# Performance work log

Hardware: AMD Instinct MI355X
Metric: run time of the kernel (lower is better)

The kernel has to match this reference:

```python
import jax, jax.numpy as jnp
import numpy as np

VARIANCES = jnp.array([0.1, 0.1, 0.2, 0.2], jnp.float32)
TOTAL_LABELS = 81
MAX_TOTAL = 200        # max_total_size (also max_output_size_per_class)
SCORE_T = 0.5          # score_threshold
IOU_T = 0.5            # tf combined_non_max_suppression default iou_threshold


def setup_inputs() -> dict:
    key = jax.random.key(0)
    k1, k2, k3, k4 = jax.random.split(key, 4)
    B, N, C = 8, 1000, TOTAL_LABELS
    # valid normalized RoIs: y1,x1 in [0,0.7), h,w in [0.01,0.31)
    yx1 = jax.random.uniform(k1, (B, N, 2), jnp.float32) * 0.7
    hw = jax.random.uniform(k2, (B, N, 2), jnp.float32) * 0.3 + 0.01
    roi_bboxes = jnp.concatenate([yx1, yx1 + hw], axis=-1)  # [y1,x1,y2,x2]
    pred_deltas = jax.random.normal(k3, (B, N, C * 4), jnp.float32) * 0.5
    pred_label_probs = jax.random.uniform(k4, (B, N, C), jnp.float32)
    return {"roi_bboxes": roi_bboxes, "pred_deltas": pred_deltas,
            "pred_label_probs": pred_label_probs}


def _decode(rois, deltas):
    # rois: [..., 4] (y1,x1,y2,x2); deltas: [..., 4] (dy,dx,dh,dw)
    h = rois[..., 2] - rois[..., 0]
    w = rois[..., 3] - rois[..., 1]
    cy = rois[..., 0] + 0.5 * h
    cx = rois[..., 1] + 0.5 * w
    ncy = deltas[..., 0] * h + cy
    ncx = deltas[..., 1] * w + cx
    nh = jnp.exp(deltas[..., 2]) * h
    nw = jnp.exp(deltas[..., 3]) * w
    return jnp.stack([ncy - 0.5 * nh, ncx - 0.5 * nw,
                      ncy + 0.5 * nh, ncx + 0.5 * nw], axis=-1)


def _nms_lane(boxes, scores):
    # greedy per-class NMS over one (batch, class) lane. boxes [N,4], scores [N]
    N = boxes.shape[0]
    order = jnp.argsort(-scores)
    b = boxes[order]
    s = scores[order]
    area = (b[:, 2] - b[:, 0]) * (b[:, 3] - b[:, 1])
    idx = jnp.arange(N)

    def body(i, keep):
        bi = b[i]
        iy1 = jnp.maximum(bi[0], b[:, 0])
        ix1 = jnp.maximum(bi[1], b[:, 1])
        iy2 = jnp.minimum(bi[2], b[:, 2])
        ix2 = jnp.minimum(bi[3], b[:, 3])
        inter = jnp.maximum(iy2 - iy1, 0.0) * jnp.maximum(ix2 - ix1, 0.0)
        iou = inter / (area[i] + area - inter + 1e-8)
        suppress = keep[i] & (iou > IOU_T) & (idx > i)
        return keep & ~suppress

    keep0 = s > SCORE_T                       # score filtering before NMS
    keep = jax.lax.fori_loop(0, N, body, keep0)
    keep = keep & (jnp.cumsum(keep) <= MAX_TOTAL)  # max_output_size_per_class
    return b, jnp.where(keep, s, 0.0)          # boxes in score order, masked scores


def _forward(roi_bboxes, pred_deltas, pred_label_probs):
    B, N, _ = pred_deltas.shape
    C = TOTAL_LABELS
    deltas = pred_deltas.reshape(B, N, C, 4) * VARIANCES
    boxes = _decode(roi_bboxes[:, :, None, :], deltas)          # [B,N,C,4]
    bg = jnp.argmax(pred_label_probs, axis=-1)[..., None] == 0  # background rows
    scores = jnp.where(bg, 0.0, pred_label_probs)               # [B,N,C]

    boxes_t = boxes.transpose(0, 2, 1, 3)   # [B,C,N,4]
    scores_t = scores.transpose(0, 2, 1)    # [B,C,N]
    b_s, s_s = jax.vmap(jax.vmap(_nms_lane))(boxes_t, scores_t)

    flat_s = s_s.reshape(B, C * N)
    flat_b = b_s.reshape(B, C * N, 4)
    cls = jnp.broadcast_to(jnp.arange(C)[:, None], (C, N)).reshape(C * N)

    top_s, top_i = jax.lax.top_k(flat_s, MAX_TOTAL)             # combined top-k
    top_b = jnp.take_along_axis(flat_b, top_i[..., None], axis=1)
    top_c = cls[top_i]

    valid = top_s > 0.0
    final_b = jnp.clip(jnp.where(valid[..., None], top_b, 0.0), 0.0, 1.0)
    final_c = jnp.where(valid, top_c, 0).astype(jnp.float32)
    final_s = jnp.where(valid, top_s, 0.0)
    return final_b, final_c, final_s


def reference(roi_bboxes, pred_deltas, pred_label_probs):
    return _forward(roi_bboxes, pred_deltas, pred_label_probs)
```

## Files before the change

### kernel.cpp

```cpp
#include <hip/hip_runtime.h>

#define NROI 1000
#define NCLS 81
#define NB   8
#define NLANE (NB*NCLS)
#define MAXM 1024
#define MAXKEEP 200
#define SCORE_T 0.5f
#define NT 512
#define NW 8
#define HBITS 13
#define HSIZE (1<<HBITS)
#define SCAP 1024

typedef unsigned long long u64;
typedef unsigned int u32;


__device__ __forceinline__ void decode_box(const float* __restrict__ roi,
                                           const float* __restrict__ dl,
                                           float& oy1, float& ox1,
                                           float& oy2, float& ox2) {
#pragma clang fp contract(off)
  float y1 = roi[0], x1 = roi[1], y2 = roi[2], x2 = roi[3];
  float h = y2 - y1;
  float w = x2 - x1;
  float cy = y1 + 0.5f * h;
  float cx = x1 + 0.5f * w;
  float d0 = dl[0] * 0.1f;
  float d1 = dl[1] * 0.1f;
  float d2 = dl[2] * 0.2f;
  float d3 = dl[3] * 0.2f;
  float ncy = d0 * h + cy;
  float ncx = d1 * w + cx;
  float nh = expf(d2) * h;
  float nw = expf(d3) * w;
  oy1 = ncy - 0.5f * nh;
  ox1 = ncx - 0.5f * nw;
  oy2 = ncy + 0.5f * nh;
  ox2 = ncx + 0.5f * nw;
}

__device__ __forceinline__ float area_f(float4 bx) {
#pragma clang fp contract(off)
  return (bx.z - bx.x) * (bx.w - bx.y);
}

__device__ __forceinline__ bool hit_f(float4 bi, float ia, float4 bj, float ja) {
#pragma clang fp contract(off)
  float yy1 = fmaxf(bi.x, bj.x);
  float xx1 = fmaxf(bi.y, bj.y);
  float yy2 = fminf(bi.z, bj.z);
  float xx2 = fminf(bi.w, bj.w);
  float ih = fmaxf(yy2 - yy1, 0.0f);
  float iw = fmaxf(xx2 - xx1, 0.0f);
  float inter = ih * iw;
  float den = ia + ja;
  den = den - inter;
  den = den + 1e-8f;
  return (inter + inter) > den;
}

__device__ __forceinline__ u64 pack_key(u32 sbits, int flat, int n) {
  return ((u64)sbits << 32) | ((u64)(131071 - flat) << 15) | ((u64)n << 5);
}

__global__ __launch_bounds__(256) void bg_kernel(const float* __restrict__ probs,
                                                 int* __restrict__ bg) {
  int row = blockIdx.x * 4 + (threadIdx.x >> 6);
  int lane = threadIdx.x & 63;
  if (row >= NB * NROI) return;
  const float* p = probs + (size_t)row * NCLS;
  float m = -1e30f;
  for (int idx = 1 + lane; idx < NCLS; idx += 64) m = fmaxf(m, p[idx]);
  for (int off = 32; off; off >>= 1) m = fmaxf(m, __shfl_xor(m, off));
  if (lane == 0) bg[row] = (p[0] >= m) ? 1 : 0;
}

__global__ __launch_bounds__(NT) void gather_nms_kernel(
    const float* __restrict__ roi, const float* __restrict__ deltas,
    const float* __restrict__ probs, const int* __restrict__ bg,
    int* __restrict__ keep_count, u64* __restrict__ lane_key,
    int* __restrict__ bhist) {
  int lane = (blockIdx.x % 8) * NCLS + blockIdx.x / 8;
  int b = lane / NCLS, c = lane % NCLS;
  int tid = threadIdx.x;
  int w = tid >> 6, l = tid & 63;

  __shared__ alignas(16) char smem[26624];
  float4* sbox   = (float4*)smem;
  u64*    skeyU  = (u64*)smem;
  u64*    skeyB  = (u64*)(smem + 8192);
  u64*    skey   = (u64*)(smem + 16384);
  int*    bcnt   = (int*)(smem + 24576);
  int*    bstart = (int*)(smem + 25600);
  __shared__ u64 hmask8[NW][64];
  __shared__ u64 suppm8[NW];
  __shared__ u64 keepmask[16];
  __shared__ int scount, segbase[16];

  if (tid == 0) scount = 0;
  if (tid < 256) bcnt[tid] = 0;
  __syncthreads();

  for (int base_n = 0; base_n < NROI; base_n += NT) {
    int n = base_n + tid;
    bool cand = false;
    float s = 0.0f;
    if (n < NROI) {
      int row = b * NROI + n;
      s = probs[(size_t)row * NCLS + c];
      cand = (s > SCORE_T) && (bg[row] == 0);
    }
    u64 bal = __ballot(cand);
    int wb = 0;
    if (l == 0) wb = atomicAdd(&scount, (int)__popcll(bal));
    wb = __shfl(wb, 0);
    if (cand) {
      int off = (int)__popcll(bal & ((1ull << l) - 1ull));
      u32 sb = __float_as_uint(s);
      skeyU[wb + off] = ((u64)sb << 32) | (u64)(0xFFFFFFFFu - (u32)n);
      atomicAdd(&bcnt[(sb >> 15) & 255], 1);
    }
  }
  __syncthreads();
  int M = scount;
  int nchunks = (M + 63) >> 6;

  if (w == 0) {
    int d0 = 4 * l, d1 = d0 + 1, d2 = d0 + 2, d3 = d0 + 3;
    int c0 = bcnt[255 - d0], c1 = bcnt[255 - d1];
    int c2 = bcnt[255 - d2], c3 = bcnt[255 - d3];
    int t = c0 + c1 + c2 + c3;
    int inc = t;
    for (int off = 1; off < 64; off <<= 1) {
      int v = __shfl_up(inc, off);
      if (l >= off) inc += v;
    }
    int excl = inc - t;
    int s0 = excl, s1 = excl + c0, s2 = excl + c0 + c1, s3 = excl + c0 + c1 + c2;
    bcnt[255 - d0] = s0; bstart[255 - d0] = s0;
    bcnt[255 - d1] = s1; bstart[255 - d1] = s1;
    bcnt[255 - d2] = s2; bstart[255 - d2] = s2;
    bcnt[255 - d3] = s3; bstart[255 - d3] = s3;
  }
  __syncthreads();

  for (int p = tid; p < M; p += NT) {
    u64 k = skeyU[p];
    int bkt = (int)((k >> 47) & 255);
    int pos = atomicAdd(&bcnt[bkt], 1);
    skeyB[pos] = k;
  }
  __syncthreads();

  for (int p = tid; p < M; p += NT) {
    u64 k = skeyB[p];
    int bkt = (int)((k >> 47) & 255);
    int st = bstart[bkt], en = bcnt[bkt];
    int r = st;
    for (int q = st; q < en; ++q) r += (skeyB[q] > k) ? 1 : 0;
    skey[r] = k;
  }
  if (tid < 16) {
    int rem = M - (tid << 6);
    keepmask[tid] = (rem >= 64) ? ~0ull : ((rem <= 0) ? 0ull : ((1ull << rem) - 1ull));
  }
  __syncthreads();

  if (w == 7 && nchunks > 0) {
    u64 k = skey[l];
    int nn = (int)(0xFFFFFFFFu - (u32)(k & 0xFFFFFFFFull));
    int row = b * NROI + ((l < M) ? nn : 0);
    float by1, bx1, by2, bx2;
    decode_box(roi + (size_t)row * 4, deltas + ((size_t)row * NCLS + c) * 4,
               by1, bx1, by2, bx2);
    sbox[l] = make_float4(by1, bx1, by2, bx2);
  }
  __syncthreads();

  int kc = 0;
  const u64 stridemask = 0x0101010101010101ull << w;
  const u64 low = (1ull << l) - 1ull;
  for (int ck = 0; ck < nchunks; ++ck) {
    int start = ck << 6;
    float4 bj = sbox[start + l];
    float ja = area_f(bj);

    {
      u64 part = 0;
#pragma unroll
      for (int r = 0; r < 8; ++r) {
        int i = (w << 3) + r;
        float4 bi = sbox[start + i];
        float ia = area_f(bi);
        if (hit_f(bi, ia, bj, ja)) part |= (1ull << i);
      }
      hmask8[w][l] = part;
    }

    {
      bool supp = false;
      for (int q = 0; q < ck; ++q) {
        u64 mq = keepmask[q] & stridemask;
        while (mq) {
          int i = __ffsll((unsigned long long)mq) - 1;
          mq &= mq - 1;
          float4 bi = sbox[(q << 6) + i];
          float ia = area_f(bi);
          supp |= hit_f(bi, ia, bj, ja);
        }
      }
      u64 sb = __ballot(supp);
      if (l == 0) suppm8[w] = sb;
    }

    if (w == 7 && ck + 1 < nchunks) {
      int p = ((ck + 1) << 6) + l;
      u64 k = skey[p];
      int nn = (int)(0xFFFFFFFFu - (u32)(k & 0xFFFFFFFFull));
      int row = b * NROI + ((p < M) ? nn : 0);
      float by1, bx1, by2, bx2;
      decode_box(roi + (size_t)row * 4, deltas + ((size_t)row * NCLS + c) * 4,
                 by1, bx1, by2, bx2);
      sbox[p] = make_float4(by1, bx1, by2, bx2);
    }
    __syncthreads();

    u64 rowm = hmask8[0][l] | hmask8[1][l] | hmask8[2][l] | hmask8[3][l]
             | hmask8[4][l] | hmask8[5][l] | hmask8[6][l] | hmask8[7][l];
    u64 sall = suppm8[0] | suppm8[1] | suppm8[2] | suppm8[3]
             | suppm8[4] | suppm8[5] | suppm8[6] | suppm8[7];
    int rem0 = M - start;
    u64 alive = (rem0 >= 64) ? ~0ull : ((rem0 <= 0) ? 0ull : ((1ull << rem0) - 1ull));
    u64 und = alive & ~sall;
    u64 kept = 0;
    while (und) {
      bool isu = (und >> l) & 1;
      bool su = isu && ((rowm & kept & low) != 0ull);
      bool ke = isu && ((rowm & (kept | und) & low) == 0ull);
      u64 sm = __ballot(su);
      u64 km2 = __ballot(ke);
      kept |= km2;
      und &= ~(sm | km2);
    }
    if (tid == 0) keepmask[ck] = kept;
    kc += (int)__popcll(kept);
    if (kc >= MAXKEEP) break;
    __syncthreads();
  }
  __syncthreads();

  if (tid < 16) {
    int acc = 0;
    for (int i = 0; i < tid; ++i) acc += (int)__popcll(keepmask[i]);
    segbase[tid] = acc;
  }
  __syncthreads();
  int total = segbase[15] + (int)__popcll(keepmask[15]);
  for (int s = 0; s < 2; ++s) {
    int seg = (w << 1) + s;
    u64 word = keepmask[seg];
    int p = (seg << 6) + l;
    if ((word >> l) & 1) {
      int rank = segbase[seg] + (int)__popcll(word & ((1ull << l) - 1ull));
      if (rank < MAXKEEP) {
        u64 k = skey[p];
        u32 sbits = (u32)(k >> 32);
        int n = (int)(0xFFFFFFFFu - (u32)(k & 0xFFFFFFFFull));
        lane_key[(size_t)lane * MAXKEEP + rank] = pack_key(sbits, c * NROI + p, n);
        atomicAdd(&bhist[b * HSIZE + (int)((sbits >> 10) & (HSIZE - 1))], 1);
      }
    }
  }
  if (tid == 0) keep_count[lane] = min(total, MAXKEEP);
}

__global__ __launch_bounds__(512) void merge_kernel(
    const float* __restrict__ roi, const float* __restrict__ deltas,
    const int* __restrict__ keep_count, const u64* __restrict__ lane_key,
    const int* __restrict__ bhist,
    float* __restrict__ out_b, float* __restrict__ out_c, float* __restrict__ out_s) {
  int b = blockIdx.x;
  int tid = threadIdx.x;
  int w = tid >> 6, l = tid & 63;

  __shared__ int hist[HSIZE];
  __shared__ int csum[256];
  __shared__ int cnts[NCLS];
  __shared__ int tb_sh, scnt_sh;
  __shared__ u64 surv[SCAP];

  for (int i = tid; i < HSIZE; i += 512) hist[i] = bhist[b * HSIZE + i];
  for (int i = tid; i < NCLS; i += 512) cnts[i] = keep_count[b * NCLS + i];
  if (tid == 0) { tb_sh = 0; scnt_sh = 0; }
  __syncthreads();

  int base = tid * 32;
  if (tid < 256) {
    int psum = 0;
    for (int i = 0; i < 32; ++i) psum += hist[base + i];
    csum[tid] = psum;
  }
  __syncthreads();
  if (w == 0) {
    int c0 = csum[4 * l], c1 = csum[4 * l + 1], c2 = csum[4 * l + 2], c3 = csum[4 * l + 3];
    int t = c0 + c1 + c2 + c3;
    int acc = t;
    for (int off = 1; off < 64; off <<= 1) {
      int v = __shfl_down(acc, off);
      if (l + off < 64) acc += v;
    }
    int below = acc - t;
    csum[4 * l + 3] = below + c3;
    csum[4 * l + 2] = below + c3 + c2;
    csum[4 * l + 1] = below + c3 + c2 + c1;
    csum[4 * l + 0] = below + t;
  }
  __syncthreads();
  if (tid < 256) {
    int acc = (tid < 255) ? csum[tid + 1] : 0;
    int local_tb = -1;
    for (int i = 31; i >= 0; --i) {
      acc += hist[base + i];
      if (acc >= MAXKEEP && local_tb < 0) local_tb = base + i;
    }
    if (local_tb >= 0) atomicMax(&tb_sh, local_tb);
  }
  __syncthreads();
  int tb = tb_sh;

  for (int s = tid; s < NCLS * MAXKEEP; s += 512) {
    int c = s / MAXKEEP, h = s % MAXKEEP;
    if (h < cnts[c]) {
      u64 k = lane_key[((size_t)(b * NCLS + c)) * MAXKEEP + h];
      u32 sb = (u32)(k >> 32);
      if ((int)((sb >> 10) & (HSIZE - 1)) >= tb) {
        int pos = atomicAdd(&scnt_sh, 1);
        if (pos < SCAP) surv[pos] = k;
      }
    }
  }
  __syncthreads();
  int scnt = min(scnt_sh, SCAP);
  int size = 2;
  while (size < scnt) size <<= 1;
  for (int i = scnt + tid; i < size; i += 512) surv[i] = 0ull;
  __syncthreads();

  for (int k2 = 2; k2 <= size; k2 <<= 1) {
    for (int j = k2 >> 1; j > 0; j >>= 1) {
      for (int i = tid; i < size; i += 512) {
        int ixj = i ^ j;
        if (ixj > i) {
          u64 a = surv[i], bb = surv[ixj];
          bool swp = ((i & k2) == 0) ? (a < bb) : (a > bb);
          if (swp) { surv[i] = bb; surv[ixj] = a; }
        }
      }
      __syncthreads();
    }
  }

  for (int t = tid; t < MAXKEEP; t += 512) {
    size_t ob = ((size_t)b * MAXKEEP + t) * 4;
    if (t < scnt) {
      u64 k = surv[t];
      int flat = 131071 - (int)((k >> 15) & 0x1FFFF);
      int c = flat / NROI;
      int n = (int)((k >> 5) & 0x3FF);
      int row = b * NROI + n;
      float by1, bx1, by2, bx2;
      decode_box(roi + (size_t)row * 4, deltas + ((size_t)row * NCLS + c) * 4,
                 by1, bx1, by2, bx2);
      out_b[ob + 0] = fminf(fmaxf(by1, 0.0f), 1.0f);
      out_b[ob + 1] = fminf(fmaxf(bx1, 0.0f), 1.0f);
      out_b[ob + 2] = fminf(fmaxf(by2, 0.0f), 1.0f);
      out_b[ob + 3] = fminf(fmaxf(bx2, 0.0f), 1.0f);
      out_c[b * MAXKEEP + t] = (float)c;
      out_s[b * MAXKEEP + t] = __uint_as_float((u32)(k >> 32));
    } else {
      out_b[ob + 0] = 0.0f; out_b[ob + 1] = 0.0f;
      out_b[ob + 2] = 0.0f; out_b[ob + 3] = 0.0f;
      out_c[b * MAXKEEP + t] = 0.0f;
      out_s[b * MAXKEEP + t] = 0.0f;
    }
  }
}

extern "C" void kernel_launch(void* const* d_in, const int* in_sizes, int n_in,
                              void* d_out, int out_size, void* d_ws, size_t ws_size,
                              hipStream_t stream) {
  const float* roi    = (const float*)d_in[0];
  const float* deltas = (const float*)d_in[1];
  const float* probs  = (const float*)d_in[2];

  char* ws = (char*)d_ws;
  int* bg         = (int*)(ws);
  int* keep_count = (int*)(ws + 32768);
  int* bhist      = (int*)(ws + 40960);
  u64* lane_key   = (u64*)(ws + 40960 + 262144);

  float* out_b = (float*)d_out;
  float* out_c = out_b + NB * MAXKEEP * 4;
  float* out_s = out_c + NB * MAXKEEP;

  hipMemsetAsync(bhist, 0, NB * HSIZE * sizeof(int), stream);
  bg_kernel<<<(NB * NROI + 3) / 4, 256, 0, stream>>>(probs, bg);
  gather_nms_kernel<<<NLANE, NT, 0, stream>>>(roi, deltas, probs, bg,
                                              keep_count, lane_key, bhist);
  merge_kernel<<<NB, 512, 0, stream>>>(roi, deltas, keep_count, lane_key, bhist,
                                       out_b, out_c, out_s);
}
```

Baseline: 72.33 us.

## Replace bitonic sort in merge with histogram bucket scatter and rank-by-count

The merge kernel no longer bitonic-sorts the surviving keys. It builds suffix offsets from the score histogram, scatters each survivor into its bucket region with atomics, and computes each key's final rank by counting larger keys within its own bucket, then writes outputs directly at that rank. The hipMemsetAsync of the histogram is folded into bg_kernel to remove one launch. This removes the many barrier-separated sort passes, at the cost of per-bucket quadratic comparisons when a bucket holds many keys. It also relies on bucket ordering matching key ordering.

```diff
diff --git a/kernel.cpp b/kernel.cpp
--- a/kernel.cpp
+++ b/kernel.cpp
@@ -66,7 +66,13 @@
 }
 
 __global__ __launch_bounds__(256) void bg_kernel(const float* __restrict__ probs,
-                                                 int* __restrict__ bg) {
+                                                 int* __restrict__ bg,
+                                                 int* __restrict__ bhist) {
+  if (blockIdx.x < 64) {
+    int base = blockIdx.x * 1024 + threadIdx.x;
+#pragma unroll
+    for (int r = 0; r < 4; ++r) bhist[base + (r << 8)] = 0;
+  }
   int row = blockIdx.x * 4 + (threadIdx.x >> 6);
   int lane = threadIdx.x & 63;
   if (row >= NB * NROI) return;
@@ -286,86 +292,85 @@
   int w = tid >> 6, l = tid & 63;
 
   __shared__ int hist[HSIZE];
+  __shared__ int hsuf[HSIZE];
+  __shared__ int hcur[HSIZE];
   __shared__ int csum[256];
   __shared__ int cnts[NCLS];
-  __shared__ int tb_sh, scnt_sh;
+  __shared__ int total_sh, scnt_sh;
   __shared__ u64 surv[SCAP];
 
   for (int i = tid; i < HSIZE; i += 512) hist[i] = bhist[b * HSIZE + i];
   for (int i = tid; i < NCLS; i += 512) cnts[i] = keep_count[b * NCLS + i];
-  if (tid == 0) { tb_sh = 0; scnt_sh = 0; }
-  __syncthreads();
-
-  int base = tid * 32;
+  if (tid == 0) scnt_sh = 0;
+  for (int t = tid; t < MAXKEEP; t += 512) {
+    size_t ob = ((size_t)b * MAXKEEP + t) * 4;
+    out_b[ob + 0] = 0.0f; out_b[ob + 1] = 0.0f;
+    out_b[ob + 2] = 0.0f; out_b[ob + 3] = 0.0f;
+    out_c[b * MAXKEEP + t] = 0.0f;
+    out_s[b * MAXKEEP + t] = 0.0f;
+  }
+  __syncthreads();
+
   if (tid < 256) {
+    int base = tid * 32;
     int psum = 0;
     for (int i = 0; i < 32; ++i) psum += hist[base + i];
     csum[tid] = psum;
   }
   __syncthreads();
   if (w == 0) {
-    int c0 = csum[4 * l], c1 = csum[4 * l + 1], c2 = csum[4 * l + 2], c3 = csum[4 * l + 3];
+    int g0 = 4 * l;
+    int c0 = csum[g0], c1 = csum[g0 + 1], c2 = csum[g0 + 2], c3 = csum[g0 + 3];
     int t = c0 + c1 + c2 + c3;
     int acc = t;
     for (int off = 1; off < 64; off <<= 1) {
       int v = __shfl_down(acc, off);
       if (l + off < 64) acc += v;
     }
-    int below = acc - t;
-    csum[4 * l + 3] = below + c3;
-    csum[4 * l + 2] = below + c3 + c2;
-    csum[4 * l + 1] = below + c3 + c2 + c1;
-    csum[4 * l + 0] = below + t;
+    if (l == 0) total_sh = acc;
+    int above = acc - t;
+    csum[g0 + 3] = above;
+    csum[g0 + 2] = above + c3;
+    csum[g0 + 1] = above + c3 + c2;
+    csum[g0 + 0] = above + c3 + c2 + c1;
   }
   __syncthreads();
   if (tid < 256) {
-    int acc = (tid < 255) ? csum[tid + 1] : 0;
-    int local_tb = -1;
+    int base = tid * 32;
+    int acc = csum[tid];
     for (int i = 31; i >= 0; --i) {
+      hsuf[base + i] = acc;
+      hcur[base + i] = acc;
       acc += hist[base + i];
-      if (acc >= MAXKEEP && local_tb < 0) local_tb = base + i;
-    }
-    if (local_tb >= 0) atomicMax(&tb_sh, local_tb);
-  }
-  __syncthreads();
-  int tb = tb_sh;
+    }
+  }
+  __syncthreads();
+  int total = total_sh;
+  int valid = (total < MAXKEEP) ? total : MAXKEEP;
 
   for (int s = tid; s < NCLS * MAXKEEP; s += 512) {
     int c = s / MAXKEEP, h = s % MAXKEEP;
     if (h < cnts[c]) {
       u64 k = lane_key[((size_t)(b * NCLS + c)) * MAXKEEP + h];
-      u32 sb = (u32)(k >> 32);
-      if ((int)((sb >> 10) & (HSIZE - 1)) >= tb) {
-        int pos = atomicAdd(&scnt_sh, 1);
-        if (pos < SCAP) surv[pos] = k;
+      int bkt = (int)((k >> 42) & (HSIZE - 1));
+      if (hsuf[bkt] < MAXKEEP) {
+        int pos = atomicAdd(&hcur[bkt], 1);
+        if (pos < SCAP) { surv[pos] = k; atomicAdd(&scnt_sh, 1); }
       }
     }
   }
   __syncthreads();
   int scnt = min(scnt_sh, SCAP);
-  int size = 2;
-  while (size < scnt) size <<= 1;
-  for (int i = scnt + tid; i < size; i += 512) surv[i] = 0ull;
-  __syncthreads();
-
-  for (int k2 = 2; k2 <= size; k2 <<= 1) {
-    for (int j = k2 >> 1; j > 0; j >>= 1) {
-      for (int i = tid; i < size; i += 512) {
-        int ixj = i ^ j;
-        if (ixj > i) {
-          u64 a = surv[i], bb = surv[ixj];
-          bool swp = ((i & k2) == 0) ? (a < bb) : (a > bb);
-          if (swp) { surv[i] = bb; surv[ixj] = a; }
-        }
-      }
-      __syncthreads();
-    }
-  }
-
-  for (int t = tid; t < MAXKEEP; t += 512) {
-    size_t ob = ((size_t)b * MAXKEEP + t) * 4;
-    if (t < scnt) {
-      u64 k = surv[t];
+
+  for (int p = tid; p < scnt; p += 512) {
+    u64 k = surv[p];
+    int bkt = (int)((k >> 42) & (HSIZE - 1));
+    int st = hsuf[bkt];
+    int en = st + hist[bkt];
+    if (en > SCAP) en = SCAP;
+    int r = st;
+    for (int q = st; q < en; ++q) r += (surv[q] > k) ? 1 : 0;
+    if (r < valid) {
       int flat = 131071 - (int)((k >> 15) & 0x1FFFF);
       int c = flat / NROI;
       int n = (int)((k >> 5) & 0x3FF);
@@ -373,17 +378,13 @@
       float by1, bx1, by2, bx2;
       decode_box(roi + (size_t)row * 4, deltas + ((size_t)row * NCLS + c) * 4,
                  by1, bx1, by2, bx2);
+      size_t ob = ((size_t)b * MAXKEEP + r) * 4;
       out_b[ob + 0] = fminf(fmaxf(by1, 0.0f), 1.0f);
       out_b[ob + 1] = fminf(fmaxf(bx1, 0.0f), 1.0f);
       out_b[ob + 2] = fminf(fmaxf(by2, 0.0f), 1.0f);
       out_b[ob + 3] = fminf(fmaxf(bx2, 0.0f), 1.0f);
-      out_c[b * MAXKEEP + t] = (float)c;
-      out_s[b * MAXKEEP + t] = __uint_as_float((u32)(k >> 32));
-    } else {
-      out_b[ob + 0] = 0.0f; out_b[ob + 1] = 0.0f;
-      out_b[ob + 2] = 0.0f; out_b[ob + 3] = 0.0f;
-      out_c[b * MAXKEEP + t] = 0.0f;
-      out_s[b * MAXKEEP + t] = 0.0f;
+      out_c[b * MAXKEEP + r] = (float)c;
+      out_s[b * MAXKEEP + r] = __uint_as_float((u32)(k >> 32));
     }
   }
 }
@@ -405,8 +406,7 @@
   float* out_c = out_b + NB * MAXKEEP * 4;
   float* out_s = out_c + NB * MAXKEEP;
 
-  hipMemsetAsync(bhist, 0, NB * HSIZE * sizeof(int), stream);
-  bg_kernel<<<(NB * NROI + 3) / 4, 256, 0, stream>>>(probs, bg);
+  bg_kernel<<<(NB * NROI + 3) / 4, 256, 0, stream>>>(probs, bg, bhist);
   gather_nms_kernel<<<NLANE, NT, 0, stream>>>(roi, deltas, probs, bg,
                                               keep_count, lane_key, bhist);
   merge_kernel<<<NB, 512, 0, stream>>>(roi, deltas, keep_count, lane_key, bhist,
```

Result: faster. 66.12 us (-8.6%).
